# Kernel tuning notes

Measured on AMD Instinct MI355X. Metric: run time of the kernel, lower is better.

## Reference

```python
import jax, jax.numpy as jnp
import numpy as np

T = 2097152          # total points across all diagrams (per side)
N_DGM = 256          # number of diagrams
D_IN, D_HID, D_OUT = 2, 32, 32


def setup_inputs() -> dict:
    key = jax.random.key(0)
    ks = jax.random.split(key, 12)
    s = 0.3
    inp = {
        "points_t": jax.random.normal(ks[0], (T, D_IN), jnp.float32),
        "points_s": jax.random.normal(ks[1], (T, D_IN), jnp.float32),
        "w1_w": jax.random.normal(ks[2], (D_IN, D_HID), jnp.float32) * s,
        "w1_b": jax.random.normal(ks[3], (D_HID,), jnp.float32) * s,
        "w2_w": jax.random.normal(ks[4], (D_HID, 1), jnp.float32) * s,
        "w2_b": jax.random.normal(ks[5], (1,), jnp.float32) * s,
        "e1_w": jax.random.normal(ks[6], (D_IN, D_HID), jnp.float32) * s,
        "e1_b": jax.random.normal(ks[7], (D_HID,), jnp.float32) * s,
        "e2_w": jax.random.normal(ks[8], (D_HID, D_OUT), jnp.float32) * s,
        "e2_b": jax.random.normal(ks[9], (D_OUT,), jnp.float32) * s,
        "seg_t": jnp.sort(jax.random.randint(ks[10], (T,), 0, N_DGM, jnp.int32)),
        "seg_s": jnp.sort(jax.random.randint(ks[11], (T,), 0, N_DGM, jnp.int32)),
        "num_diagrams": N_DGM,
    }
    return inp


def _point_pool(pts, seg, w1_w, w1_b, w2_w, w2_b, e1_w, e1_b, e2_w, e2_b, n_dgm):
    # torch.nan_to_num(dgm, posinf=0)
    x = jnp.nan_to_num(pts, posinf=0.0)
    # weight MLP: Linear(2,32) -> ReLU -> Linear(32,1)
    w = jax.nn.relu(x @ w1_w + w1_b) @ w2_w + w2_b            # [T, 1]
    # embedding MLP: Linear(2,32) -> ReLU -> Linear(32,32)
    e = jax.nn.relu(x @ e1_w + e1_b) @ e2_w + e2_b            # [T, 32]
    prod = w * e                                              # [T, 32]
    sums = jax.ops.segment_sum(prod, seg, num_segments=n_dgm)               # [N, 32]
    cnts = jax.ops.segment_sum(jnp.ones((pts.shape[0], 1), prod.dtype), seg,
                               num_segments=n_dgm)                          # [N, 1]
    pooled = sums / jnp.maximum(cnts, 1.0)                    # per-diagram mean
    return pooled.reshape(-1)                                 # torch.cat -> [N*32]


def reference(points_t, points_s, w1_w, w1_b, w2_w, w2_b, e1_w, e1_b, e2_w, e2_b,
              seg_t, seg_s, num_diagrams):
    params = (w1_w, w1_b, w2_w, w2_b, e1_w, e1_b, e2_w, e2_b)
    emb_t = _point_pool(points_t, seg_t, *params, num_diagrams)
    emb_s = _point_pool(points_s, seg_s, *params, num_diagrams)
    return jnp.mean((emb_s - emb_t) ** 2)
```

## Files before the change

kernel.cpp:

```cpp
#include <hip/hip_runtime.h>

typedef float f4 __attribute__((ext_vector_type(4)));

#define NSEG 256
#define BPS 2
#define KPT 8
#define NSLOT 8
#define STRIDE (BPS * 256 * KPT)


__global__ __launch_bounds__(256) void bounds2_kernel(
    const int* __restrict__ seg_t, const int* __restrict__ seg_s,
    int* __restrict__ starts_t, int* __restrict__ starts_s, int T) {
  const int side = blockIdx.y;
  const int* seg = side ? seg_s : seg_t;
  int* starts = side ? starts_s : starts_t;
  const int gi = ((int)blockIdx.x * 256 + (int)threadIdx.x) * 16;
  if (gi >= T) return;
  const int4* v = (const int4*)(seg + gi);
  const int4 a = v[0], b = v[1], c = v[2], d = v[3];
  const int s[16] = {a.x, a.y, a.z, a.w, b.x, b.y, b.z, b.w,
                     c.x, c.y, c.z, c.w, d.x, d.y, d.z, d.w};
  int prev = (gi == 0) ? -1 : seg[gi - 1];
#pragma unroll
  for (int k = 0; k < 16; ++k) {
    for (int t = prev + 1; t <= s[k]; ++t) starts[t] = gi + k;
    prev = s[k];
  }
  if (gi + 16 >= T) {
    for (int t = prev + 1; t <= NSEG; ++t) starts[t] = T;
  }
}

__global__ __launch_bounds__(256, 4) void pool_kernel(
    const float2* __restrict__ pts_t, const float2* __restrict__ pts_s,
    const int* __restrict__ starts_t, const int* __restrict__ starts_s,
    const float* __restrict__ w1_w, const float* __restrict__ w1_b,
    const float* __restrict__ w2_w, const float* __restrict__ w2_b,
    const float* __restrict__ e1_w, const float* __restrict__ e1_b,
    float* __restrict__ part_g, float* __restrict__ part_w, int T) {
  const int side = blockIdx.z;
  const float2* pts = side ? pts_s : pts_t;
  const int* starts = side ? starts_s : starts_t;
  const int s = blockIdx.x;
  const int tid = threadIdx.x;

  __shared__ __align__(16) float wtA[8][16];
  __shared__ __align__(16) float wtB[8][12];
  __shared__ float w2b_sh;
  if (tid < 32) {
    const int q = tid >> 2, j = tid & 3, h = tid;
    wtA[q][j] = w1_w[h];
    wtA[q][4 + j] = w1_w[32 + h];
    wtA[q][8 + j] = w1_b[h];
    wtA[q][12 + j] = w2_w[h];
    wtB[q][j] = e1_w[h];
    wtB[q][4 + j] = e1_w[32 + h];
    wtB[q][8 + j] = e1_b[h];
  }
  if (tid == 0) w2b_sh = w2_b[0];
  __syncthreads();

  const int st = starts[s];
  const int en = starts[s + 1];
  const int st2 = st & ~1;
  const int total2 = en - st2;
  const int Tm2 = T - 2;
  const unsigned cnt = (unsigned)(en - st);
  const float w2b = w2b_sh;

  float ag[32];
#pragma unroll
  for (int h = 0; h < 32; ++h) ag[h] = 0.f;
  float aw = 0.f;

  for (int base = ((int)blockIdx.y * 256 + tid) * KPT; base < total2;
       base += STRIDE) {
    const int i0 = st2 + base;

    float px[KPT], py[KPT];
#pragma unroll
    for (int j = 0; j < 4; ++j) {
      int ip = i0 + 2 * j;
      ip = ip > Tm2 ? Tm2 : ip;
      const f4 q = *reinterpret_cast<const f4*>(&pts[ip]);
      px[2 * j] = q.x;
      py[2 * j] = q.y;
      px[2 * j + 1] = q.z;
      py[2 * j + 1] = q.w;
    }

    unsigned zoff = 0;
    asm volatile("" : "+v"(zoff));
    const char* wa = (const char*)(&wtA[0][0]) + zoff;
    const char* wbp = (const char*)(&wtB[0][0]) + zoff;

    float wacc[KPT];
#pragma unroll
    for (int k = 0; k < KPT; ++k) wacc[k] = 0.f;

#pragma unroll 1
    for (int q = 0; q < 8; ++q) {
      const f4 QX = *(const f4*)(wa + q * 64);
      const f4 QY = *(const f4*)(wa + q * 64 + 16);
      const f4 QB = *(const f4*)(wa + q * 64 + 32);
      const f4 QW = *(const f4*)(wa + q * 64 + 48);
#pragma unroll
      for (int k = 0; k < KPT; ++k) {
        float h0 = fmaf(px[k], QX.x, fmaf(py[k], QY.x, QB.x));
        wacc[k] = fmaf(fmaxf(h0, 0.f), QW.x, wacc[k]);
        float h1 = fmaf(px[k], QX.y, fmaf(py[k], QY.y, QB.y));
        wacc[k] = fmaf(fmaxf(h1, 0.f), QW.y, wacc[k]);
        float h2 = fmaf(px[k], QX.z, fmaf(py[k], QY.z, QB.z));
        wacc[k] = fmaf(fmaxf(h2, 0.f), QW.z, wacc[k]);
        float h3 = fmaf(px[k], QX.w, fmaf(py[k], QY.w, QB.w));
        wacc[k] = fmaf(fmaxf(h3, 0.f), QW.w, wacc[k]);
      }
    }

    float wv[KPT];
#pragma unroll
    for (int k = 0; k < KPT; ++k) {
      float w = wacc[k] + w2b;
      const bool valid = (unsigned)(i0 + k - st) < cnt;
      w = valid ? w : 0.f;
      wv[k] = w;
      aw += w;
    }

#pragma unroll
    for (int q = 0; q < 8; ++q) {
      const f4 EX = *(const f4*)(wbp + q * 48);
      const f4 EY = *(const f4*)(wbp + q * 48 + 16);
      const f4 EB = *(const f4*)(wbp + q * 48 + 32);
      float a0 = ag[4 * q], a1 = ag[4 * q + 1];
      float a2 = ag[4 * q + 2], a3 = ag[4 * q + 3];
#pragma unroll
      for (int k = 0; k < KPT; ++k) {
        const float e0 = fmaxf(fmaf(px[k], EX.x, fmaf(py[k], EY.x, EB.x)), 0.f);
        a0 = fmaf(wv[k], e0, a0);
        const float e1 = fmaxf(fmaf(px[k], EX.y, fmaf(py[k], EY.y, EB.y)), 0.f);
        a1 = fmaf(wv[k], e1, a1);
        const float e2 = fmaxf(fmaf(px[k], EX.z, fmaf(py[k], EY.z, EB.z)), 0.f);
        a2 = fmaf(wv[k], e2, a2);
        const float e3 = fmaxf(fmaf(px[k], EX.w, fmaf(py[k], EY.w, EB.w)), 0.f);
        a3 = fmaf(wv[k], e3, a3);
      }
      ag[4 * q] = a0;
      ag[4 * q + 1] = a1;
      ag[4 * q + 2] = a2;
      ag[4 * q + 3] = a3;
    }
  }

  float v[32];
#pragma unroll
  for (int h = 0; h < 32; ++h) v[h] = ag[h];
  const int l = tid & 63;

#define FOLD(M, HALF)                                    \
  {                                                      \
    const bool hi = (l & (M)) != 0;                      \
    _Pragma("unroll") for (int i = 0; i < (HALF); ++i) { \
      const float sent = hi ? v[i] : v[i + (HALF)];      \
      const float kept = hi ? v[i + (HALF)] : v[i];      \
      v[i] = kept + __shfl_xor(sent, (M));               \
    }                                                    \
  }
  FOLD(1, 16)
  FOLD(2, 8)
  FOLD(4, 4)
  FOLD(8, 2)
  FOLD(16, 1)
#undef FOLD
  v[0] += __shfl_xor(v[0], 32);
  const int h = ((l & 1) << 4) | ((l & 2) << 2) | (l & 4) | ((l & 8) >> 2) |
                ((l & 16) >> 4);

#pragma unroll
  for (int m = 1; m < 64; m <<= 1) aw += __shfl_xor(aw, m);

  const int slot = (int)blockIdx.y * 4 + (tid >> 6);
  const int unit = side * NSEG + s;
  if (l < 32) part_g[(unit * NSLOT + slot) * 32 + h] = v[0];
  if (l == 0) part_w[unit * NSLOT + slot] = aw;
}

__global__ __launch_bounds__(256) void finishA_kernel(
    const float* __restrict__ part_g, const float* __restrict__ part_w,
    float* __restrict__ emb_g, float* __restrict__ emb_w) {
  const int gu = blockIdx.x * 8 + (threadIdx.x >> 5);
  const int h = threadIdx.x & 31;
  const float* pg = part_g + gu * NSLOT * 32 + h;
  float sum = 0.f;
#pragma unroll
  for (int k = 0; k < NSLOT; ++k) sum += pg[k * 32];
  emb_g[gu * 32 + h] = sum;
  if (h == 0) {
    const float* pw = part_w + gu * NSLOT;
    float sw = 0.f;
#pragma unroll
    for (int k = 0; k < NSLOT; ++k) sw += pw[k];
    emb_w[gu] = sw;
  }
}

__global__ __launch_bounds__(256) void finishB_kernel(
    const float* __restrict__ emb_g, const float* __restrict__ emb_w,
    const int* __restrict__ starts_t, const int* __restrict__ starts_s,
    const float* __restrict__ e2_w, const float* __restrict__ e2_b,
    float* __restrict__ out) {
  const int s = threadIdx.x;
  __shared__ float e2s[32][33];
  __shared__ float e2bs[32];
  for (int k = threadIdx.x; k < 1024; k += 256) e2s[k >> 5][k & 31] = e2_w[k];
  if (threadIdx.x < 32) e2bs[threadIdx.x] = e2_b[threadIdx.x];
  __syncthreads();

  const float* gt = &emb_g[s * 32];
  const float* gs = &emb_g[(NSEG + s) * 32];
  const float awt = emb_w[s];
  const float aws = emb_w[NSEG + s];
  const float ct = fmaxf((float)(starts_t[s + 1] - starts_t[s]), 1.f);
  const float cs = fmaxf((float)(starts_s[s + 1] - starts_s[s]), 1.f);

  float gtl[32], gsl[32];
#pragma unroll
  for (int h = 0; h < 32; ++h) {
    gtl[h] = gt[h];
    gsl[h] = gs[h];
  }

  float part = 0.f;
#pragma unroll
  for (int o = 0; o < 32; ++o) {
    float pt = awt * e2bs[o];
    float ps = aws * e2bs[o];
#pragma unroll
    for (int h = 0; h < 32; ++h) {
      const float w = e2s[h][o];
      pt = fmaf(gtl[h], w, pt);
      ps = fmaf(gsl[h], w, ps);
    }
    pt /= ct;
    ps /= cs;
    const float d = ps - pt;
    part = fmaf(d, d, part);
  }

  __shared__ float red[256];
  red[threadIdx.x] = part;
  __syncthreads();
  for (int k = 128; k > 0; k >>= 1) {
    if (threadIdx.x < k) red[threadIdx.x] += red[threadIdx.x + k];
    __syncthreads();
  }
  if (threadIdx.x == 0) out[0] = red[0] / (float)(NSEG * 32);
}

extern "C" void kernel_launch(void* const* d_in, const int* in_sizes, int n_in,
                              void* d_out, int out_size, void* d_ws,
                              size_t ws_size, hipStream_t stream) {
  const float2* pts_t = (const float2*)d_in[0];
  const float2* pts_s = (const float2*)d_in[1];
  const float* w1_w = (const float*)d_in[2];
  const float* w1_b = (const float*)d_in[3];
  const float* w2_w = (const float*)d_in[4];
  const float* w2_b = (const float*)d_in[5];
  const float* e1_w = (const float*)d_in[6];
  const float* e1_b = (const float*)d_in[7];
  const float* e2_w = (const float*)d_in[8];
  const float* e2_b = (const float*)d_in[9];
  const int* seg_t = (const int*)d_in[10];
  const int* seg_s = (const int*)d_in[11];
  const int T = in_sizes[0] / 2;

  char* ws = (char*)d_ws;
  int* starts_t = (int*)ws;
  int* starts_s = (int*)(ws + 1028);
  float* part_g = (float*)(ws + 4096);
  float* part_w = (float*)(ws + 528384);
  float* emb_g = (float*)(ws + 544768);
  float* emb_w = (float*)(ws + 610304);

  dim3 gA((T / 16 + 255) / 256, 2, 1);
  bounds2_kernel<<<gA, 256, 0, stream>>>(seg_t, seg_s, starts_t, starts_s, T);

  dim3 gB(NSEG, BPS, 2);
  pool_kernel<<<gB, 256, 0, stream>>>(pts_t, pts_s, starts_t, starts_s, w1_w,
                                      w1_b, w2_w, w2_b, e1_w, e1_b, part_g,
                                      part_w, T);

  finishA_kernel<<<64, 256, 0, stream>>>(part_g, part_w, emb_g, emb_w);
  finishB_kernel<<<1, 256, 0, stream>>>(emb_g, emb_w, starts_t, starts_s, e2_w,
                                        e2_b, (float*)d_out);
}
```

Baseline: 52.80 us.

## Fuse finish kernels into pool kernel via atomics and last-block reduction

Each pool block now atomically adds its per-wave partial sums directly into the per-diagram embedding buffers, replacing the partial-slot writes. A global counter picks the last finishing block, which applies the second embedding layer and computes the final MSE, so the two separate finish kernels go away. The bounds kernel zeroes the accumulators and the counter. Separately, the weight-MLP loop over hidden quads is now fully unrolled. This removes two kernel launches and a round trip through workspace, at the cost of float atomics (order-dependent summation), a threadfence per block, and extra register pressure from the unroll.

```diff
diff --git a/kernel.cpp b/kernel.cpp
--- a/kernel.cpp
+++ b/kernel.cpp
@@ -5,13 +5,21 @@
 #define NSEG 256
 #define BPS 2
 #define KPT 8
-#define NSLOT 8
 #define STRIDE (BPS * 256 * KPT)
+#define NBLK_POOL (NSEG * BPS * 2)
 
 
 __global__ __launch_bounds__(256) void bounds2_kernel(
     const int* __restrict__ seg_t, const int* __restrict__ seg_s,
-    int* __restrict__ starts_t, int* __restrict__ starts_s, int T) {
+    int* __restrict__ starts_t, int* __restrict__ starts_s,
+    int* __restrict__ counter, float* __restrict__ emb_g,
+    float* __restrict__ emb_w, int T) {
+  if (blockIdx.y == 0) {
+    const int t = (int)blockIdx.x * 256 + (int)threadIdx.x;
+    if (t < 16384) emb_g[t] = 0.f;
+    if (t < 512) emb_w[t] = 0.f;
+    if (t == 0) *counter = 0;
+  }
   const int side = blockIdx.y;
   const int* seg = side ? seg_s : seg_t;
   int* starts = side ? starts_s : starts_t;
@@ -32,13 +40,15 @@
   }
 }
 
-__global__ __launch_bounds__(256, 4) void pool_kernel(
+__global__ __launch_bounds__(256, 4) void fused_kernel(
     const float2* __restrict__ pts_t, const float2* __restrict__ pts_s,
     const int* __restrict__ starts_t, const int* __restrict__ starts_s,
     const float* __restrict__ w1_w, const float* __restrict__ w1_b,
     const float* __restrict__ w2_w, const float* __restrict__ w2_b,
     const float* __restrict__ e1_w, const float* __restrict__ e1_b,
-    float* __restrict__ part_g, float* __restrict__ part_w, int T) {
+    const float* __restrict__ e2_w, const float* __restrict__ e2_b,
+    float* __restrict__ emb_g, float* __restrict__ emb_w,
+    int* __restrict__ counter, float* __restrict__ out, int T) {
   const int side = blockIdx.z;
   const float2* pts = side ? pts_s : pts_t;
   const int* starts = side ? starts_s : starts_t;
@@ -48,6 +58,7 @@
   __shared__ __align__(16) float wtA[8][16];
   __shared__ __align__(16) float wtB[8][12];
   __shared__ float w2b_sh;
+  __shared__ int last_flag;
   if (tid < 32) {
     const int q = tid >> 2, j = tid & 3, h = tid;
     wtA[q][j] = w1_w[h];
@@ -99,7 +110,7 @@
 #pragma unroll
     for (int k = 0; k < KPT; ++k) wacc[k] = 0.f;
 
-#pragma unroll 1
+#pragma unroll
     for (int q = 0; q < 8; ++q) {
       const f4 QX = *(const f4*)(wa + q * 64);
       const f4 QY = *(const f4*)(wa + q * 64 + 16);
@@ -180,82 +191,68 @@
 #pragma unroll
   for (int m = 1; m < 64; m <<= 1) aw += __shfl_xor(aw, m);
 
-  const int slot = (int)blockIdx.y * 4 + (tid >> 6);
   const int unit = side * NSEG + s;
-  if (l < 32) part_g[(unit * NSLOT + slot) * 32 + h] = v[0];
-  if (l == 0) part_w[unit * NSLOT + slot] = aw;
-}
-
-__global__ __launch_bounds__(256) void finishA_kernel(
-    const float* __restrict__ part_g, const float* __restrict__ part_w,
-    float* __restrict__ emb_g, float* __restrict__ emb_w) {
-  const int gu = blockIdx.x * 8 + (threadIdx.x >> 5);
-  const int h = threadIdx.x & 31;
-  const float* pg = part_g + gu * NSLOT * 32 + h;
-  float sum = 0.f;
-#pragma unroll
-  for (int k = 0; k < NSLOT; ++k) sum += pg[k * 32];
-  emb_g[gu * 32 + h] = sum;
-  if (h == 0) {
-    const float* pw = part_w + gu * NSLOT;
-    float sw = 0.f;
-#pragma unroll
-    for (int k = 0; k < NSLOT; ++k) sw += pw[k];
-    emb_w[gu] = sw;
-  }
-}
-
-__global__ __launch_bounds__(256) void finishB_kernel(
-    const float* __restrict__ emb_g, const float* __restrict__ emb_w,
-    const int* __restrict__ starts_t, const int* __restrict__ starts_s,
-    const float* __restrict__ e2_w, const float* __restrict__ e2_b,
-    float* __restrict__ out) {
-  const int s = threadIdx.x;
-  __shared__ float e2s[32][33];
-  __shared__ float e2bs[32];
-  for (int k = threadIdx.x; k < 1024; k += 256) e2s[k >> 5][k & 31] = e2_w[k];
-  if (threadIdx.x < 32) e2bs[threadIdx.x] = e2_b[threadIdx.x];
+  if (l < 32) atomicAdd(&emb_g[unit * 32 + h], v[0]);
+  if (l == 0) atomicAdd(&emb_w[unit], aw);
+  __threadfence();
   __syncthreads();
-
-  const float* gt = &emb_g[s * 32];
-  const float* gs = &emb_g[(NSEG + s) * 32];
-  const float awt = emb_w[s];
-  const float aws = emb_w[NSEG + s];
-  const float ct = fmaxf((float)(starts_t[s + 1] - starts_t[s]), 1.f);
-  const float cs = fmaxf((float)(starts_s[s + 1] - starts_s[s]), 1.f);
-
-  float gtl[32], gsl[32];
-#pragma unroll
-  for (int h = 0; h < 32; ++h) {
-    gtl[h] = gt[h];
-    gsl[h] = gs[h];
-  }
-
-  float part = 0.f;
-#pragma unroll
-  for (int o = 0; o < 32; ++o) {
-    float pt = awt * e2bs[o];
-    float ps = aws * e2bs[o];
-#pragma unroll
-    for (int h = 0; h < 32; ++h) {
-      const float w = e2s[h][o];
-      pt = fmaf(gtl[h], w, pt);
-      ps = fmaf(gsl[h], w, ps);
-    }
-    pt /= ct;
-    ps /= cs;
-    const float d = ps - pt;
-    part = fmaf(d, d, part);
-  }
-
-  __shared__ float red[256];
-  red[threadIdx.x] = part;
+  if (tid == 0) {
+    const int old = __hip_atomic_fetch_add(counter, 1, __ATOMIC_ACQ_REL,
+                                           __HIP_MEMORY_SCOPE_AGENT);
+    last_flag = (old == NBLK_POOL - 1);
+  }
   __syncthreads();
-  for (int k = 128; k > 0; k >>= 1) {
-    if (threadIdx.x < k) red[threadIdx.x] += red[threadIdx.x + k];
+  if (!last_flag) return;
+
+  {
+    __shared__ float e2s[32][33];
+    __shared__ float e2bs[32];
+    __shared__ float red[256];
+    for (int k = tid; k < 1024; k += 256) e2s[k >> 5][k & 31] = e2_w[k];
+    if (tid < 32) e2bs[tid] = e2_b[tid];
     __syncthreads();
-  }
-  if (threadIdx.x == 0) out[0] = red[0] / (float)(NSEG * 32);
+
+    const int sg = tid;
+    float gtl[32], gsl[32];
+#pragma unroll
+    for (int hh = 0; hh < 32; ++hh) {
+      gtl[hh] = __hip_atomic_load(&emb_g[sg * 32 + hh], __ATOMIC_RELAXED,
+                                  __HIP_MEMORY_SCOPE_AGENT);
+      gsl[hh] = __hip_atomic_load(&emb_g[(NSEG + sg) * 32 + hh],
+                                  __ATOMIC_RELAXED, __HIP_MEMORY_SCOPE_AGENT);
+    }
+    const float awt = __hip_atomic_load(&emb_w[sg], __ATOMIC_RELAXED,
+                                        __HIP_MEMORY_SCOPE_AGENT);
+    const float aws = __hip_atomic_load(&emb_w[NSEG + sg], __ATOMIC_RELAXED,
+                                        __HIP_MEMORY_SCOPE_AGENT);
+    const float ct = fmaxf((float)(starts_t[sg + 1] - starts_t[sg]), 1.f);
+    const float cs = fmaxf((float)(starts_s[sg + 1] - starts_s[sg]), 1.f);
+
+    float part = 0.f;
+#pragma unroll
+    for (int o = 0; o < 32; ++o) {
+      float pt = awt * e2bs[o];
+      float ps = aws * e2bs[o];
+#pragma unroll
+      for (int hh = 0; hh < 32; ++hh) {
+        const float w = e2s[hh][o];
+        pt = fmaf(gtl[hh], w, pt);
+        ps = fmaf(gsl[hh], w, ps);
+      }
+      pt /= ct;
+      ps /= cs;
+      const float d = ps - pt;
+      part = fmaf(d, d, part);
+    }
+
+    red[tid] = part;
+    __syncthreads();
+    for (int k = 128; k > 0; k >>= 1) {
+      if (tid < k) red[tid] += red[tid + k];
+      __syncthreads();
+    }
+    if (tid == 0) out[0] = red[0] / (float)(NSEG * 32);
+  }
 }
 
 extern "C" void kernel_launch(void* const* d_in, const int* in_sizes, int n_in,
@@ -278,20 +275,17 @@
   char* ws = (char*)d_ws;
   int* starts_t = (int*)ws;
   int* starts_s = (int*)(ws + 1028);
-  float* part_g = (float*)(ws + 4096);
-  float* part_w = (float*)(ws + 528384);
-  float* emb_g = (float*)(ws + 544768);
-  float* emb_w = (float*)(ws + 610304);
+  int* counter = (int*)(ws + 2056);
+  float* emb_g = (float*)(ws + 4096);
+  float* emb_w = (float*)(ws + 69632);
 
   dim3 gA((T / 16 + 255) / 256, 2, 1);
-  bounds2_kernel<<<gA, 256, 0, stream>>>(seg_t, seg_s, starts_t, starts_s, T);
+  bounds2_kernel<<<gA, 256, 0, stream>>>(seg_t, seg_s, starts_t, starts_s,
+                                         counter, emb_g, emb_w, T);
 
   dim3 gB(NSEG, BPS, 2);
-  pool_kernel<<<gB, 256, 0, stream>>>(pts_t, pts_s, starts_t, starts_s, w1_w,
-                                      w1_b, w2_w, w2_b, e1_w, e1_b, part_g,
-                                      part_w, T);
-
-  finishA_kernel<<<64, 256, 0, stream>>>(part_g, part_w, emb_g, emb_w);
-  finishB_kernel<<<1, 256, 0, stream>>>(emb_g, emb_w, starts_t, starts_s, e2_w,
-                                        e2_b, (float*)d_out);
+  fused_kernel<<<gB, 256, 0, stream>>>(pts_t, pts_s, starts_t, starts_s, w1_w,
+                                       w1_b, w2_w, w2_b, e1_w, e1_b, e2_w,
+                                       e2_b, emb_g, emb_w, counter,
+                                       (float*)d_out, T);
 }
```

Result: slower. 135.1 us (+155.8%).
